# Performance work log

Hardware: AMD Instinct MI355X
Metric: run time of the kernel (lower is better)

## Reference

```python
import jax, jax.numpy as jnp
import numpy as np

B, H, T = 16, 2048, 512


def setup_inputs() -> dict:
    key = jax.random.key(0)
    ks = jax.random.split(key, 9)
    s = 1.0 / np.sqrt(H)
    return {
        "traj_z": jax.random.normal(ks[0], (B, H), dtype=jnp.float32),
        "traj_input": jax.random.normal(ks[1], (B, T), dtype=jnp.float32),
        "w_ih": jax.random.uniform(ks[2], (3 * H, 1), jnp.float32, -s, s),
        "b_ih": jax.random.uniform(ks[3], (3 * H,), jnp.float32, -s, s),
        "w_hh": jax.random.uniform(ks[4], (3 * H, H), jnp.float32, -s, s),
        "b_hh": jax.random.uniform(ks[5], (3 * H,), jnp.float32, -s, s),
        "w_traj": jax.random.uniform(ks[6], (1, H), jnp.float32, -s, s),
        "b_traj": jax.random.uniform(ks[7], (1,), jnp.float32, -s, s),
        "timesteps": T,
    }


def reference(traj_z, traj_input, w_ih, b_ih, w_hh, b_hh, w_traj, b_traj, timesteps):
    # epoch = inf -> teacher-forcing mask is all zeros -> blend is identity.
    x0 = traj_input[:, 0:1]  # [B, 1]

    def step(carry, _):
        h, x = carry
        gi = x @ w_ih.T + b_ih            # [B, 3H]
        gh = h @ w_hh.T + b_hh            # [B, 3H]
        i_r, i_z, i_n = jnp.split(gi, 3, axis=-1)
        h_r, h_z, h_n = jnp.split(gh, 3, axis=-1)
        r = jax.nn.sigmoid(i_r + h_r)
        z = jax.nn.sigmoid(i_z + h_z)
        n = jnp.tanh(i_n + r * h_n)
        h_new = (1.0 - z) * n + z * h     # GRUCell update
        x_new = h_new @ w_traj.T + b_traj + x  # residual linear head, [B, 1]
        return (h_new, x_new), x_new

    _, ys = jax.lax.scan(step, (traj_z, x0), None, length=timesteps)
    return jnp.transpose(ys, (1, 0, 2))  # [B, T, 1]
```

## Files before the change

### kernel.cpp

```cpp
#include <hip/hip_runtime.h>
#include <stdint.h>
#include <math.h>

#define Hdim   2048
#define Bdim   16
#define Tsteps 512
#define NWG    128
#define TPB    256
#define KC     16
#define NCHUNK 16
#define FLAGSTRIDE 32
#define HBYTES (Bdim * Hdim * 2)

typedef __attribute__((ext_vector_type(8))) short short8_t;
typedef __attribute__((ext_vector_type(4))) float f32x4;
typedef __attribute__((ext_vector_type(4))) unsigned int u32x4;

__device__ __forceinline__ short f2bf(float x) {
  uint32_t u = __builtin_bit_cast(uint32_t, x);
  u += 0x7fffu + ((u >> 16) & 1u);
  return (short)(u >> 16);
}

__device__ __forceinline__ short8_t load8_bf(const float* __restrict__ p) {
  short8_t r;
#pragma unroll
  for (int j = 0; j < 8; ++j) r[j] = f2bf(p[j]);
  return r;
}

__device__ __forceinline__ void publish(uint32_t* flags, int wg, int tid, uint32_t n) {
  asm volatile("s_waitcnt vmcnt(0)" ::: "memory");
  __syncthreads();
  if (tid == 0)
    __hip_atomic_store(flags + wg * FLAGSTRIDE, n, __ATOMIC_RELAXED, __HIP_MEMORY_SCOPE_AGENT);
}

__device__ __forceinline__ void wait_quarter(const uint32_t* flags, int wave, int lane, uint32_t n) {
  if (lane < 32) {
    const uint32_t* f = flags + (wave * 32 + lane) * FLAGSTRIDE;
    while (__hip_atomic_load(f, __ATOMIC_RELAXED, __HIP_MEMORY_SCOPE_AGENT) < n) {
      __builtin_amdgcn_s_sleep(1);
    }
  }
  __builtin_amdgcn_sched_barrier(0);
}

__device__ __forceinline__ void publish_h(uint32_t* hbuf32, int buf,
                                          int eb, int ekc, int ecol, float h_own) {
  uint32_t mybits = (uint32_t)(uint16_t)f2bf(h_own);
  uint32_t n1 = (uint32_t)__shfl_xor((int)mybits, 1, 64);
  uint32_t a  = (mybits & 0xffffu) | (n1 << 16);
  uint32_t b  = (uint32_t)__shfl_xor((int)a, 2, 64);
  uint32_t c4 = (uint32_t)__shfl_xor((int)a, 4, 64);
  uint32_t d  = (uint32_t)__shfl_xor((int)b, 4, 64);
  if ((ekc & 7) == 0) {
    u32x4 q; q.x = a; q.y = b; q.z = c4; q.w = d;
    char* dst = (char*)hbuf32 + (size_t)buf * HBYTES
              + ((size_t)(ecol >> 3) * 256 + (size_t)eb * 16);
    asm volatile("global_store_dwordx4 %0, %1, off sc0 sc1" :: "v"(dst), "v"(q) : "memory");
  }
}

__global__ void __launch_bounds__(TPB, 1) traj_kernel(
    const float* __restrict__ traj_z, const float* __restrict__ traj_input,
    const float* __restrict__ w_ih, const float* __restrict__ b_ih,
    const float* __restrict__ w_hh, const float* __restrict__ b_hh,
    const float* __restrict__ w_traj, const float* __restrict__ b_traj,
    float* __restrict__ out, uint32_t* __restrict__ hbuf32, uint32_t* __restrict__ flags)
{
  const int tid  = threadIdx.x;
  const int wg   = blockIdx.x;
  const int wave = tid >> 6;
  const int lane = tid & 63;
  const int ln16 = lane & 15;
  const int quad = lane >> 4;
  const int colbase = wg * KC;
  const int kwave   = wave * (Hdim / 4);

  __shared__ float s_red[4][3][16][16];
  __shared__ float s_x3[4][16];

  short8_t wf0[NCHUNK], wf1[NCHUNK], wf2[NCHUNK], wt[NCHUNK];
#pragma unroll
  for (int c = 0; c < NCHUNK; ++c) {
    const int k0 = kwave + c * 32 + quad * 8;
    wf0[c] = load8_bf(w_hh + (size_t)(0 * Hdim + colbase + ln16) * Hdim + k0);
    wf1[c] = load8_bf(w_hh + (size_t)(1 * Hdim + colbase + ln16) * Hdim + k0);
    wf2[c] = load8_bf(w_hh + (size_t)(2 * Hdim + colbase + ln16) * Hdim + k0);
    short8_t g = {0, 0, 0, 0, 0, 0, 0, 0};
    if (ln16 == 0) g = load8_bf(w_traj + k0);
    wt[c] = g;
  }

  const int eb   = tid >> 4;
  const int ekc  = tid & 15;
  const int ecol = colbase + ekc;
  const float wr = w_ih[ecol], wz = w_ih[Hdim + ecol], wn = w_ih[2 * Hdim + ecol];
  const float br = b_ih[ecol] + b_hh[ecol];
  const float bz = b_ih[Hdim + ecol] + b_hh[Hdim + ecol];
  const float bin = b_ih[2 * Hdim + ecol];
  const float bhn = b_hh[2 * Hdim + ecol];
  const float bt  = b_traj[0];
  float h_own = traj_z[eb * Hdim + ecol];
  float x_reg = traj_input[eb * Tsteps];

  publish_h(hbuf32, 0, eb, ekc, ecol, h_own);
  publish(flags, wg, tid, 1);

  for (int i = 0; i <= Tsteps; ++i) {
    wait_quarter(flags, wave, lane, (uint32_t)(i + 1));

    asm volatile("s_waitcnt vmcnt(0)" ::: "memory");

    const char* hbase = (const char*)hbuf32 + (size_t)(i & 1) * HBYTES
                      + (size_t)(kwave >> 5) * 1024 + (size_t)lane * 16;
    short8_t af[NCHUNK];
#pragma unroll
    for (int c = 0; c < NCHUNK; ++c) {
      asm volatile("global_load_dwordx4 %0, %1, off sc0 sc1"
                   : "=v"(af[c]) : "v"(hbase + (size_t)c * 1024));
    }

    f32x4 a0 = {0.f, 0.f, 0.f, 0.f}, a1 = a0, a2 = a0, a3 = a0;

#define MFMA_GROUP(G, VM)                                                      \
    asm volatile("s_waitcnt vmcnt(" #VM ")" ::: "memory");                     \
    __builtin_amdgcn_sched_barrier(0);                                         \
    _Pragma("unroll")                                                          \
    for (int c = (G) * 4; c < (G) * 4 + 4; ++c) {                              \
      a0 = __builtin_amdgcn_mfma_f32_16x16x32_bf16(af[c], wf0[c], a0, 0, 0, 0);\
      a1 = __builtin_amdgcn_mfma_f32_16x16x32_bf16(af[c], wf1[c], a1, 0, 0, 0);\
      a2 = __builtin_amdgcn_mfma_f32_16x16x32_bf16(af[c], wf2[c], a2, 0, 0, 0);\
      a3 = __builtin_amdgcn_mfma_f32_16x16x32_bf16(af[c], wt[c],  a3, 0, 0, 0);\
    }

    MFMA_GROUP(0, 12)
    MFMA_GROUP(1, 8)
    MFMA_GROUP(2, 4)
    MFMA_GROUP(3, 0)
#undef MFMA_GROUP

#pragma unroll
    for (int r = 0; r < 4; ++r) {
      const int m = quad * 4 + r;
      s_red[wave][0][m][ln16] = a0[r];
      s_red[wave][1][m][ln16] = a1[r];
      s_red[wave][2][m][ln16] = a2[r];
    }
    if (ln16 == 0) {
#pragma unroll
      for (int r = 0; r < 4; ++r) s_x3[wave][quad * 4 + r] = a3[r];
    }
    __syncthreads();

    if (i > 0) {
      const float xd = ((s_x3[0][eb] + s_x3[1][eb]) + s_x3[2][eb]) + s_x3[3][eb];
      x_reg += xd + bt;
      if (wg == 0 && ekc == 0) out[eb * Tsteps + (i - 1)] = x_reg;
    }
    if (i == Tsteps) break;

    const float gr = ((s_red[0][0][eb][ekc] + s_red[1][0][eb][ekc]) + s_red[2][0][eb][ekc]) + s_red[3][0][eb][ekc];
    const float gz = ((s_red[0][1][eb][ekc] + s_red[1][1][eb][ekc]) + s_red[2][1][eb][ekc]) + s_red[3][1][eb][ekc];
    const float gn = ((s_red[0][2][eb][ekc] + s_red[1][2][eb][ekc]) + s_red[2][2][eb][ekc]) + s_red[3][2][eb][ekc];
    const float x  = x_reg;
    const float rr = 1.f / (1.f + expf(-(x * wr + br + gr)));
    const float zz = 1.f / (1.f + expf(-(x * wz + bz + gz)));
    const float nn = tanhf(x * wn + bin + rr * (gn + bhn));
    h_own = (1.f - zz) * nn + zz * h_own;

    publish_h(hbuf32, (i + 1) & 1, eb, ekc, ecol, h_own);
    publish(flags, wg, tid, (uint32_t)(i + 2));
  }
}

extern "C" void kernel_launch(void* const* d_in, const int* in_sizes, int n_in,
                              void* d_out, int out_size, void* d_ws, size_t ws_size,
                              hipStream_t stream) {
  const float* traj_z     = (const float*)d_in[0];
  const float* traj_input = (const float*)d_in[1];
  const float* w_ih   = (const float*)d_in[2];
  const float* b_ih   = (const float*)d_in[3];
  const float* w_hh   = (const float*)d_in[4];
  const float* b_hh   = (const float*)d_in[5];
  const float* w_traj = (const float*)d_in[6];
  const float* b_traj = (const float*)d_in[7];
  float* out = (float*)d_out;

  uint8_t*  ws    = (uint8_t*)d_ws;
  uint32_t* flags = (uint32_t*)ws;
  uint32_t* hbuf  = (uint32_t*)(ws + NWG * FLAGSTRIDE * 4);

  (void)hipMemsetAsync(flags, 0, NWG * FLAGSTRIDE * 4, stream);
  hipLaunchKernelGGL(traj_kernel, dim3(NWG), dim3(TPB), 0, stream,
                     traj_z, traj_input, w_ih, b_ih, w_hh, b_hh, w_traj, b_traj,
                     out, hbuf, flags);
}
```

Measured before the change: 1.681 ms.

## Use a 513-slot ring buffer so hidden-state reads can skip cache-bypass bits

```diff
diff --git a/kernel.cpp b/kernel.cpp
--- a/kernel.cpp
+++ b/kernel.cpp
@@ -11,6 +11,8 @@
 #define NCHUNK 16
 #define FLAGSTRIDE 32
 #define HBYTES (Bdim * Hdim * 2)
+#define NBUF   513
+#define PSTRIDE 31
 
 typedef __attribute__((ext_vector_type(8))) short short8_t;
 typedef __attribute__((ext_vector_type(4))) float f32x4;
@@ -46,8 +48,7 @@
   __builtin_amdgcn_sched_barrier(0);
 }
 
-__device__ __forceinline__ void publish_h(uint32_t* hbuf32, int buf,
-                                          int eb, int ekc, int ecol, float h_own) {
+__device__ __forceinline__ void publish_h(char* dstbase, int eb, int ekc, int ecol, float h_own) {
   uint32_t mybits = (uint32_t)(uint16_t)f2bf(h_own);
   uint32_t n1 = (uint32_t)__shfl_xor((int)mybits, 1, 64);
   uint32_t a  = (mybits & 0xffffu) | (n1 << 16);
@@ -56,73 +57,44 @@
   uint32_t d  = (uint32_t)__shfl_xor((int)b, 4, 64);
   if ((ekc & 7) == 0) {
     u32x4 q; q.x = a; q.y = b; q.z = c4; q.w = d;
-    char* dst = (char*)hbuf32 + (size_t)buf * HBYTES
-              + ((size_t)(ecol >> 3) * 256 + (size_t)eb * 16);
+    char* dst = dstbase + ((size_t)(ecol >> 3) * 256 + (size_t)eb * 16);
     asm volatile("global_store_dwordx4 %0, %1, off sc0 sc1" :: "v"(dst), "v"(q) : "memory");
   }
 }
 
-__global__ void __launch_bounds__(TPB, 1) traj_kernel(
-    const float* __restrict__ traj_z, const float* __restrict__ traj_input,
-    const float* __restrict__ w_ih, const float* __restrict__ b_ih,
-    const float* __restrict__ w_hh, const float* __restrict__ b_hh,
-    const float* __restrict__ w_traj, const float* __restrict__ b_traj,
-    float* __restrict__ out, uint32_t* __restrict__ hbuf32, uint32_t* __restrict__ flags)
-{
-  const int tid  = threadIdx.x;
-  const int wg   = blockIdx.x;
-  const int wave = tid >> 6;
-  const int lane = tid & 63;
-  const int ln16 = lane & 15;
-  const int quad = lane >> 4;
-  const int colbase = wg * KC;
-  const int kwave   = wave * (Hdim / 4);
-
-  __shared__ float s_red[4][3][16][16];
-  __shared__ float s_x3[4][16];
-
-  short8_t wf0[NCHUNK], wf1[NCHUNK], wf2[NCHUNK], wt[NCHUNK];
-#pragma unroll
-  for (int c = 0; c < NCHUNK; ++c) {
-    const int k0 = kwave + c * 32 + quad * 8;
-    wf0[c] = load8_bf(w_hh + (size_t)(0 * Hdim + colbase + ln16) * Hdim + k0);
-    wf1[c] = load8_bf(w_hh + (size_t)(1 * Hdim + colbase + ln16) * Hdim + k0);
-    wf2[c] = load8_bf(w_hh + (size_t)(2 * Hdim + colbase + ln16) * Hdim + k0);
-    short8_t g = {0, 0, 0, 0, 0, 0, 0, 0};
-    if (ln16 == 0) g = load8_bf(w_traj + k0);
-    wt[c] = g;
-  }
-
-  const int eb   = tid >> 4;
-  const int ekc  = tid & 15;
-  const int ecol = colbase + ekc;
-  const float wr = w_ih[ecol], wz = w_ih[Hdim + ecol], wn = w_ih[2 * Hdim + ecol];
-  const float br = b_ih[ecol] + b_hh[ecol];
-  const float bz = b_ih[Hdim + ecol] + b_hh[Hdim + ecol];
-  const float bin = b_ih[2 * Hdim + ecol];
-  const float bhn = b_hh[2 * Hdim + ecol];
-  const float bt  = b_traj[0];
-  float h_own = traj_z[eb * Hdim + ecol];
+#define KERNEL_PROLOGUE                                                          \
+  const int tid  = threadIdx.x;                                                  \
+  const int wg   = blockIdx.x;                                                   \
+  const int wave = tid >> 6;                                                     \
+  const int lane = tid & 63;                                                     \
+  const int ln16 = lane & 15;                                                    \
+  const int quad = lane >> 4;                                                    \
+  const int colbase = wg * KC;                                                   \
+  const int kwave   = wave * (Hdim / 4);                                         \
+  __shared__ float s_red[4][3][16][16];                                          \
+  __shared__ float s_x3[4][16];                                                  \
+  short8_t wf0[NCHUNK], wf1[NCHUNK], wf2[NCHUNK], wt[NCHUNK];                    \
+  _Pragma("unroll")                                                              \
+  for (int c = 0; c < NCHUNK; ++c) {                                             \
+    const int k0 = kwave + c * 32 + quad * 8;                                    \
+    wf0[c] = load8_bf(w_hh + (size_t)(0 * Hdim + colbase + ln16) * Hdim + k0);   \
+    wf1[c] = load8_bf(w_hh + (size_t)(1 * Hdim + colbase + ln16) * Hdim + k0);   \
+    wf2[c] = load8_bf(w_hh + (size_t)(2 * Hdim + colbase + ln16) * Hdim + k0);   \
+    short8_t g = {0, 0, 0, 0, 0, 0, 0, 0};                                       \
+    if (ln16 == 0) g = load8_bf(w_traj + k0);                                    \
+    wt[c] = g;                                                                   \
+  }                                                                              \
+  const int eb   = tid >> 4;                                                     \
+  const int ekc  = tid & 15;                                                     \
+  const int ecol = colbase + ekc;                                                \
+  const float wr = w_ih[ecol], wz = w_ih[Hdim + ecol], wn = w_ih[2 * Hdim + ecol];\
+  const float br = b_ih[ecol] + b_hh[ecol];                                      \
+  const float bz = b_ih[Hdim + ecol] + b_hh[Hdim + ecol];                        \
+  const float bin = b_ih[2 * Hdim + ecol];                                       \
+  const float bhn = b_hh[2 * Hdim + ecol];                                       \
+  const float bt  = b_traj[0];                                                   \
+  float h_own = traj_z[eb * Hdim + ecol];                                        \
   float x_reg = traj_input[eb * Tsteps];
-
-  publish_h(hbuf32, 0, eb, ekc, ecol, h_own);
-  publish(flags, wg, tid, 1);
-
-  for (int i = 0; i <= Tsteps; ++i) {
-    wait_quarter(flags, wave, lane, (uint32_t)(i + 1));
-
-    asm volatile("s_waitcnt vmcnt(0)" ::: "memory");
-
-    const char* hbase = (const char*)hbuf32 + (size_t)(i & 1) * HBYTES
-                      + (size_t)(kwave >> 5) * 1024 + (size_t)lane * 16;
-    short8_t af[NCHUNK];
-#pragma unroll
-    for (int c = 0; c < NCHUNK; ++c) {
-      asm volatile("global_load_dwordx4 %0, %1, off sc0 sc1"
-                   : "=v"(af[c]) : "v"(hbase + (size_t)c * 1024));
-    }
-
-    f32x4 a0 = {0.f, 0.f, 0.f, 0.f}, a1 = a0, a2 = a0, a3 = a0;
 
 #define MFMA_GROUP(G, VM)                                                      \
     asm volatile("s_waitcnt vmcnt(" #VM ")" ::: "memory");                     \
@@ -135,43 +107,114 @@
       a3 = __builtin_amdgcn_mfma_f32_16x16x32_bf16(af[c], wt[c],  a3, 0, 0, 0);\
     }
 
+#define KERNEL_TAIL                                                              \
+    _Pragma("unroll")                                                            \
+    for (int r = 0; r < 4; ++r) {                                                \
+      const int m = quad * 4 + r;                                                \
+      s_red[wave][0][m][ln16] = a0[r];                                           \
+      s_red[wave][1][m][ln16] = a1[r];                                           \
+      s_red[wave][2][m][ln16] = a2[r];                                           \
+    }                                                                            \
+    if (ln16 == 0) {                                                             \
+      _Pragma("unroll")                                                          \
+      for (int r = 0; r < 4; ++r) s_x3[wave][quad * 4 + r] = a3[r];              \
+    }                                                                            \
+    __syncthreads();                                                             \
+    if (i > 0) {                                                                 \
+      const float xd = ((s_x3[0][eb] + s_x3[1][eb]) + s_x3[2][eb]) + s_x3[3][eb];\
+      x_reg += xd + bt;                                                          \
+    }                                                                            \
+    if (i == Tsteps) {                                                           \
+      if (wg == 0 && ekc == 0) out[eb * Tsteps + (i - 1)] = x_reg;               \
+      break;                                                                     \
+    }                                                                            \
+    const float gr = ((s_red[0][0][eb][ekc] + s_red[1][0][eb][ekc]) + s_red[2][0][eb][ekc]) + s_red[3][0][eb][ekc]; \
+    const float gz = ((s_red[0][1][eb][ekc] + s_red[1][1][eb][ekc]) + s_red[2][1][eb][ekc]) + s_red[3][1][eb][ekc]; \
+    const float gn = ((s_red[0][2][eb][ekc] + s_red[1][2][eb][ekc]) + s_red[2][2][eb][ekc]) + s_red[3][2][eb][ekc]; \
+    const float x  = x_reg;                                                      \
+    const float rr = 1.f / (1.f + expf(-(x * wr + br + gr)));                    \
+    const float zz = 1.f / (1.f + expf(-(x * wz + bz + gz)));                    \
+    const float nn = tanhf(x * wn + bin + rr * (gn + bhn));                      \
+    h_own = (1.f - zz) * nn + zz * h_own;
+
+__global__ void __launch_bounds__(TPB, 1) traj_kernel_ring(
+    const float* __restrict__ traj_z, const float* __restrict__ traj_input,
+    const float* __restrict__ w_ih, const float* __restrict__ b_ih,
+    const float* __restrict__ w_hh, const float* __restrict__ b_hh,
+    const float* __restrict__ w_traj, const float* __restrict__ b_traj,
+    float* __restrict__ out, char* __restrict__ ring, uint32_t* __restrict__ flags)
+{
+  KERNEL_PROLOGUE
+
+  publish_h(ring , eb, ekc, ecol, h_own);
+  publish(flags, wg, tid, 1);
+
+  int rd = 0;
+  for (int i = 0; i <= Tsteps; ++i) {
+    wait_quarter(flags, wave, lane, (uint32_t)(i + 1));
+    asm volatile("s_waitcnt vmcnt(0)" ::: "memory");
+
+    const char* hbase = ring + (size_t)rd * HBYTES
+                      + (size_t)(kwave >> 5) * 1024 + (size_t)lane * 16;
+    short8_t af[NCHUNK];
+#pragma unroll
+    for (int c = 0; c < NCHUNK; ++c) {
+      asm volatile("global_load_dwordx4 %0, %1, off"
+                   : "=v"(af[c]) : "v"(hbase + (size_t)c * 1024));
+    }
+
+    f32x4 a0 = {0.f, 0.f, 0.f, 0.f}, a1 = a0, a2 = a0, a3 = a0;
     MFMA_GROUP(0, 12)
     MFMA_GROUP(1, 8)
     MFMA_GROUP(2, 4)
     MFMA_GROUP(3, 0)
-#undef MFMA_GROUP
-
+
+    KERNEL_TAIL
+
+    int wr_slot = rd + PSTRIDE; if (wr_slot >= NBUF) wr_slot -= NBUF;
+    publish_h(ring + (size_t)wr_slot * HBYTES, eb, ekc, ecol, h_own);
+    publish(flags, wg, tid, (uint32_t)(i + 2));
+    if (wg == 0 && i > 0 && ekc == 0) out[eb * Tsteps + (i - 1)] = x_reg;
+    rd = wr_slot;
+  }
+}
+
+__global__ void __launch_bounds__(TPB, 1) traj_kernel_base(
+    const float* __restrict__ traj_z, const float* __restrict__ traj_input,
+    const float* __restrict__ w_ih, const float* __restrict__ b_ih,
+    const float* __restrict__ w_hh, const float* __restrict__ b_hh,
+    const float* __restrict__ w_traj, const float* __restrict__ b_traj,
+    float* __restrict__ out, char* __restrict__ hbuf, uint32_t* __restrict__ flags)
+{
+  KERNEL_PROLOGUE
+
+  publish_h(hbuf , eb, ekc, ecol, h_own);
+  publish(flags, wg, tid, 1);
+
+  for (int i = 0; i <= Tsteps; ++i) {
+    wait_quarter(flags, wave, lane, (uint32_t)(i + 1));
+    asm volatile("s_waitcnt vmcnt(0)" ::: "memory");
+
+    const char* hbase = hbuf + (size_t)(i & 1) * HBYTES
+                      + (size_t)(kwave >> 5) * 1024 + (size_t)lane * 16;
+    short8_t af[NCHUNK];
 #pragma unroll
-    for (int r = 0; r < 4; ++r) {
-      const int m = quad * 4 + r;
-      s_red[wave][0][m][ln16] = a0[r];
-      s_red[wave][1][m][ln16] = a1[r];
-      s_red[wave][2][m][ln16] = a2[r];
-    }
-    if (ln16 == 0) {
-#pragma unroll
-      for (int r = 0; r < 4; ++r) s_x3[wave][quad * 4 + r] = a3[r];
-    }
-    __syncthreads();
-
-    if (i > 0) {
-      const float xd = ((s_x3[0][eb] + s_x3[1][eb]) + s_x3[2][eb]) + s_x3[3][eb];
-      x_reg += xd + bt;
-      if (wg == 0 && ekc == 0) out[eb * Tsteps + (i - 1)] = x_reg;
-    }
-    if (i == Tsteps) break;
-
-    const float gr = ((s_red[0][0][eb][ekc] + s_red[1][0][eb][ekc]) + s_red[2][0][eb][ekc]) + s_red[3][0][eb][ekc];
-    const float gz = ((s_red[0][1][eb][ekc] + s_red[1][1][eb][ekc]) + s_red[2][1][eb][ekc]) + s_red[3][1][eb][ekc];
-    const float gn = ((s_red[0][2][eb][ekc] + s_red[1][2][eb][ekc]) + s_red[2][2][eb][ekc]) + s_red[3][2][eb][ekc];
-    const float x  = x_reg;
-    const float rr = 1.f / (1.f + expf(-(x * wr + br + gr)));
-    const float zz = 1.f / (1.f + expf(-(x * wz + bz + gz)));
-    const float nn = tanhf(x * wn + bin + rr * (gn + bhn));
-    h_own = (1.f - zz) * nn + zz * h_own;
-
-    publish_h(hbuf32, (i + 1) & 1, eb, ekc, ecol, h_own);
+    for (int c = 0; c < NCHUNK; ++c) {
+      asm volatile("global_load_dwordx4 %0, %1, off sc0 sc1"
+                   : "=v"(af[c]) : "v"(hbase + (size_t)c * 1024));
+    }
+
+    f32x4 a0 = {0.f, 0.f, 0.f, 0.f}, a1 = a0, a2 = a0, a3 = a0;
+    MFMA_GROUP(0, 12)
+    MFMA_GROUP(1, 8)
+    MFMA_GROUP(2, 4)
+    MFMA_GROUP(3, 0)
+
+    KERNEL_TAIL
+
+    publish_h(hbuf + (size_t)((i + 1) & 1) * HBYTES, eb, ekc, ecol, h_own);
     publish(flags, wg, tid, (uint32_t)(i + 2));
+    if (wg == 0 && i > 0 && ekc == 0) out[eb * Tsteps + (i - 1)] = x_reg;
   }
 }
 
@@ -190,10 +233,18 @@
 
   uint8_t*  ws    = (uint8_t*)d_ws;
   uint32_t* flags = (uint32_t*)ws;
-  uint32_t* hbuf  = (uint32_t*)(ws + NWG * FLAGSTRIDE * 4);
+  char*     hbuf  = (char*)(ws + 16384);
 
   (void)hipMemsetAsync(flags, 0, NWG * FLAGSTRIDE * 4, stream);
-  hipLaunchKernelGGL(traj_kernel, dim3(NWG), dim3(TPB), 0, stream,
-                     traj_z, traj_input, w_ih, b_ih, w_hh, b_hh, w_traj, b_traj,
-                     out, hbuf, flags);
-}
+
+  const size_t ring_need = 16384ull + (size_t)NBUF * HBYTES;
+  if (ws_size >= ring_need) {
+    hipLaunchKernelGGL(traj_kernel_ring, dim3(NWG), dim3(TPB), 0, stream,
+                       traj_z, traj_input, w_ih, b_ih, w_hh, b_hh, w_traj, b_traj,
+                       out, hbuf, flags);
+  } else {
+    hipLaunchKernelGGL(traj_kernel_base, dim3(NWG), dim3(TPB), 0, stream,
+                       traj_z, traj_input, w_ih, b_ih, w_hh, b_hh, w_traj, b_traj,
+                       out, hbuf, flags);
+  }
+}
```

New measurement: 1.617 ms. 3.8% less time.
